# Optimization experiments

Measured on AMD Instinct MI355X. Metric: run time of the kernel, lower is better.

Reference implementation:

```python
import jax, jax.numpy as jnp
import numpy as np

HID = 128
CDIM = 128
NCH = 3
NDIM = 3


def _linear_params(key, fan_in, fan_out):
    kw, kb = jax.random.split(key)
    bound = 1.0 / np.sqrt(fan_in)
    W = jax.random.uniform(kw, (fan_in, fan_out), jnp.float32, -bound, bound)
    b = jax.random.uniform(kb, (fan_out,), jnp.float32, -bound, bound)
    return W, b


def setup_inputs() -> dict:
    key = jax.random.key(0)
    keys = jax.random.split(key, 12)
    p = jax.random.normal(keys[0], (32, 8192, NDIM), jnp.float32)
    W_pos, b_pos = _linear_params(keys[1], NDIM, 2 * HID)
    W0, b0 = _linear_params(keys[2], 2 * HID, HID)
    W1, b1 = _linear_params(keys[3], 2 * HID, HID)
    W2, b2 = _linear_params(keys[4], 2 * HID, HID)
    W3, b3 = _linear_params(keys[5], 2 * HID, HID)
    Wc, bc = _linear_params(keys[6], HID, CDIM)
    Wm0, bm0 = _linear_params(keys[7], CDIM, HID)
    Wm1, bm1 = _linear_params(keys[8], HID, HID)
    Wm2, bm2 = _linear_params(keys[9], HID, HID)
    Wp, bp = _linear_params(keys[10], HID, NCH * 3)
    return dict(p=p, W_pos=W_pos, b_pos=b_pos, W0=W0, b0=b0, W1=W1, b1=b1,
                W2=W2, b2=b2, W3=W3, b3=b3, Wc=Wc, bc=bc,
                Wm0=Wm0, bm0=bm0, Wm1=Wm1, bm1=bm1, Wm2=Wm2, bm2=bm2,
                Wp=Wp, bp=bp)


def _relu(x):
    return jnp.maximum(x, 0)


def _pool_cat(net):
    # max over points (dim=1), broadcast back and concat on features
    pooled = jnp.max(net, axis=1, keepdims=True)
    pooled = jnp.broadcast_to(pooled, net.shape)
    return jnp.concatenate([net, pooled], axis=2)  # [B, T, 2*hid]


def reference(p, W_pos, b_pos, W0, b0, W1, b1, W2, b2, W3, b3,
              Wc, bc, Wm0, bm0, Wm1, bm1, Wm2, bm2, Wp, bp):
    net = p @ W_pos + b_pos                      # [B, T, 2*hid]
    net = _relu(net) @ W0 + b0                   # [B, T, hid]
    net = _relu(_pool_cat(net)) @ W1 + b1        # [B, T, hid]
    net = _relu(_pool_cat(net)) @ W2 + b2        # [B, T, hid]
    net = _relu(_pool_cat(net)) @ W3 + b3        # [B, T, hid]
    net = jnp.max(net, axis=1)                   # [B, hid]
    net = _relu(net) @ Wc + bc                   # [B, c_dim]
    net = _relu(net) @ Wm0 + bm0
    net = _relu(net) @ Wm1 + bm1
    net = _relu(net) @ Wm2 + bm2
    net = _relu(net) @ Wp + bp                   # [B, n_channels*3]
    return net
```

## Files before the change

kernel.cpp:

```cpp
#include <hip/hip_runtime.h>


using bf16x8 = __attribute__((ext_vector_type(8))) __bf16;
using u16x8  = __attribute__((ext_vector_type(8))) unsigned short;
using f32x4  = __attribute__((ext_vector_type(4))) float;

__device__ __forceinline__ unsigned short f2bf(float x) {
  __bf16 b = (__bf16)x;
  return __builtin_bit_cast(unsigned short, b);
}

__device__ __forceinline__ f32x4 mfma16(bf16x8 a, bf16x8 b, f32x4 c) {
  return __builtin_amdgcn_mfma_f32_16x16x32_bf16(a, b, c, 0, 0, 0);
}

union FragU { unsigned short us[8]; u16x8 u; bf16x8 v; };

__global__ __launch_bounds__(256) void k_pack_all(
    const float* __restrict__ W0, const float* __restrict__ W1,
    const float* __restrict__ W2, const float* __restrict__ W3,
    unsigned short* __restrict__ Wt) {
  const int blk = blockIdx.x, t = threadIdx.x;
  const float* src; int slot; unsigned short* dst;
  if (blk < 16)      { src = W0; slot = blk * 256 + t;        dst = Wt; }
  else if (blk < 24) { src = W1; slot = (blk - 16) * 256 + t; dst = Wt + 32768; }
  else if (blk < 32) { src = W2; slot = (blk - 24) * 256 + t; dst = Wt + 49152; }
  else               { src = W3; slot = (blk - 32) * 256 + t; dst = Wt + 65536; }
  const int ks = slot >> 9, rem = slot & 511;
  const int nt = rem >> 6, lane = rem & 63;
  const int n = nt * 16 + (lane & 15);
  const int kb = ks * 32 + ((lane >> 4) << 3);
  FragU fr;
#pragma unroll
  for (int j = 0; j < 8; ++j) fr.us[j] = f2bf(src[(kb + j) * 128 + n]);
  reinterpret_cast<u16x8*>(dst)[slot] = fr.u;
}

__global__ __launch_bounds__(256) void k_layer0(
    const float* __restrict__ p, const float* __restrict__ Wpos,
    const float* __restrict__ bpos, const float* __restrict__ b0,
    const unsigned short* __restrict__ Wt0, unsigned short* __restrict__ h,
    float* __restrict__ pm) {
  __shared__ unsigned short wlsb[1024];
  __shared__ float pmaxs[2][128];
  const int t = threadIdx.x, blk = blockIdx.x;

  {
    const int m = t;
    const int phi = ((m >> 4) >> 1) * 32 + (((m & 15) >> 2) << 3) +
                    (((m >> 4) & 1) << 2) + (m & 3);
    ushort4 wv;
    wv.x = f2bf(Wpos[phi]);       wv.y = f2bf(Wpos[256 + phi]);
    wv.z = f2bf(Wpos[512 + phi]); wv.w = f2bf(bpos[phi]);
    *reinterpret_cast<ushort4*>(&wlsb[m * 4]) = wv;
  }
  __syncthreads();

  const int w = t >> 6, lane = t & 63, g = lane >> 4, c = lane & 15;
  const int rowg = w >> 1, colg = w & 1;

  FragU pf[2];
#pragma unroll
  for (int mi = 0; mi < 2; ++mi) {
#pragma unroll
    for (int j = 0; j < 8; ++j) pf[mi].us[j] = 0;
    if (g == 0) {
      const int row = blk * 64 + rowg * 32 + mi * 16 + c;
      pf[mi].us[0] = f2bf(p[row * 3 + 0]);
      pf[mi].us[1] = f2bf(p[row * 3 + 1]);
      pf[mi].us[2] = f2bf(p[row * 3 + 2]);
      pf[mi].us[3] = (unsigned short)0x3F80;
    }
  }

  f32x4 acc[2][4];
#pragma unroll
  for (int mi = 0; mi < 2; ++mi)
#pragma unroll
    for (int ntl = 0; ntl < 4; ++ntl) acc[mi][ntl] = f32x4{0.f, 0.f, 0.f, 0.f};

  const bf16x8* Bf = reinterpret_cast<const bf16x8*>(Wt0);
  const f32x4 zz = {0.f, 0.f, 0.f, 0.f};

#pragma unroll
  for (int ks = 0; ks < 8; ++ks) {
    bf16x8 B[4];
#pragma unroll
    for (int ntl = 0; ntl < 4; ++ntl)
      B[ntl] = Bf[(ks * 8 + colg * 4 + ntl) * 64 + lane];

    FragU a1_0, a1_1;
#pragma unroll
    for (int j = 0; j < 8; ++j) { a1_0.us[j] = 0; a1_1.us[j] = 0; }
    if (g == 0) {
      const ushort4 wv0 = *reinterpret_cast<const ushort4*>(&wlsb[((2 * ks) * 16 + c) * 4]);
      const ushort4 wv1 = *reinterpret_cast<const ushort4*>(&wlsb[((2 * ks + 1) * 16 + c) * 4]);
      a1_0.us[0] = wv0.x; a1_0.us[1] = wv0.y; a1_0.us[2] = wv0.z; a1_0.us[3] = wv0.w;
      a1_1.us[0] = wv1.x; a1_1.us[1] = wv1.y; a1_1.us[2] = wv1.z; a1_1.us[3] = wv1.w;
    }

#pragma unroll
    for (int mi = 0; mi < 2; ++mi) {
      const f32x4 qe0 = mfma16(a1_0.v, pf[mi].v, zz);
      const f32x4 qe1 = mfma16(a1_1.v, pf[mi].v, zz);
      FragU af;
#pragma unroll
      for (int j = 0; j < 4; ++j) af.us[j] = f2bf(fmaxf(qe0[j], 0.f));
#pragma unroll
      for (int j = 0; j < 4; ++j) af.us[4 + j] = f2bf(fmaxf(qe1[j], 0.f));
#pragma unroll
      for (int ntl = 0; ntl < 4; ++ntl)
        acc[mi][ntl] = mfma16(B[ntl], af.v, acc[mi][ntl]);
    }
  }

  unsigned short* hout = h + (size_t)blk * 8192;
#pragma unroll
  for (int ntl = 0; ntl < 4; ++ntl) {
    const int ntg = colg * 4 + ntl;
    const float4 bb = *reinterpret_cast<const float4*>(&b0[ntg * 16 + g * 4]);
    float vm[4] = {0.f, 0.f, 0.f, 0.f};
#pragma unroll
    for (int mi = 0; mi < 2; ++mi) {
      const float v0 = fmaxf(acc[mi][ntl][0] + bb.x, 0.f);
      const float v1 = fmaxf(acc[mi][ntl][1] + bb.y, 0.f);
      const float v2 = fmaxf(acc[mi][ntl][2] + bb.z, 0.f);
      const float v3 = fmaxf(acc[mi][ntl][3] + bb.w, 0.f);
      vm[0] = fmaxf(vm[0], v0); vm[1] = fmaxf(vm[1], v1);
      vm[2] = fmaxf(vm[2], v2); vm[3] = fmaxf(vm[3], v3);
      ushort4 s4;
      s4.x = f2bf(v0); s4.y = f2bf(v1); s4.z = f2bf(v2); s4.w = f2bf(v3);
      const int slot = (rowg * 2 + mi) * 256 + (ntg >> 1) * 64 +
                       ((ntg & 1) * 2 + (g >> 1)) * 16 + c;
      *reinterpret_cast<ushort4*>(&hout[slot * 8 + (g & 1) * 4]) = s4;
    }
#pragma unroll
    for (int r = 0; r < 4; ++r) {
      vm[r] = fmaxf(vm[r], __shfl_xor(vm[r], 1, 64));
      vm[r] = fmaxf(vm[r], __shfl_xor(vm[r], 2, 64));
      vm[r] = fmaxf(vm[r], __shfl_xor(vm[r], 4, 64));
      vm[r] = fmaxf(vm[r], __shfl_xor(vm[r], 8, 64));
    }
    if (c == 0) {
#pragma unroll
      for (int r = 0; r < 4; ++r) pmaxs[rowg][ntg * 16 + g * 4 + r] = vm[r];
    }
  }
  __syncthreads();
  if (t < 128) pm[(size_t)blk * 128 + t] = fmaxf(pmaxs[0][t], pmaxs[1][t]);
}

__global__ __launch_bounds__(256) void k_layer(
    const unsigned short* __restrict__ Wta, const float* __restrict__ cvec,
    unsigned short* __restrict__ h, float* __restrict__ pm, int write_h) {
  __shared__ float pmaxs[2][128];
  const int t = threadIdx.x, blk = blockIdx.x;
  const int w = t >> 6, lane = t & 63, g = lane >> 4, c = lane & 15;
  const int rowg = w >> 1, colg = w & 1;
  const int b = blk >> 6;

  f32x4 acc[4][4];
#pragma unroll
  for (int mi = 0; mi < 4; ++mi)
#pragma unroll
    for (int ntl = 0; ntl < 4; ++ntl) acc[mi][ntl] = f32x4{0.f, 0.f, 0.f, 0.f};

  const u16x8* hblk = reinterpret_cast<const u16x8*>(h) + (size_t)blk * 2048;
  const bf16x8* Bf = reinterpret_cast<const bf16x8*>(Wta);
#pragma unroll
  for (int ks = 0; ks < 4; ++ks) {
    bf16x8 B[4];
#pragma unroll
    for (int ntl = 0; ntl < 4; ++ntl)
      B[ntl] = Bf[(ks * 8 + colg * 4 + ntl) * 64 + lane];
    FragU a[4];
#pragma unroll
    for (int mi = 0; mi < 4; ++mi)
      a[mi].u = hblk[(rowg * 4 + mi) * 256 + ks * 64 + lane];
#pragma unroll
    for (int mi = 0; mi < 4; ++mi)
#pragma unroll
      for (int ntl = 0; ntl < 4; ++ntl)
        acc[mi][ntl] = mfma16(B[ntl], a[mi].v, acc[mi][ntl]);
  }

  unsigned short* hout = h + (size_t)blk * 16384;
#pragma unroll
  for (int ntl = 0; ntl < 4; ++ntl) {
    const int ntg = colg * 4 + ntl;
    const float4 bb = *reinterpret_cast<const float4*>(&cvec[b * 128 + ntg * 16 + g * 4]);
    float vm[4] = {0.f, 0.f, 0.f, 0.f};
#pragma unroll
    for (int mi = 0; mi < 4; ++mi) {
      const float v0 = fmaxf(acc[mi][ntl][0] + bb.x, 0.f);
      const float v1 = fmaxf(acc[mi][ntl][1] + bb.y, 0.f);
      const float v2 = fmaxf(acc[mi][ntl][2] + bb.z, 0.f);
      const float v3 = fmaxf(acc[mi][ntl][3] + bb.w, 0.f);
      vm[0] = fmaxf(vm[0], v0); vm[1] = fmaxf(vm[1], v1);
      vm[2] = fmaxf(vm[2], v2); vm[3] = fmaxf(vm[3], v3);
      if (write_h) {
        ushort4 s4;
        s4.x = f2bf(v0); s4.y = f2bf(v1); s4.z = f2bf(v2); s4.w = f2bf(v3);
        const int slot = (rowg * 4 + mi) * 256 + (ntg >> 1) * 64 +
                         ((ntg & 1) * 2 + (g >> 1)) * 16 + c;
        *reinterpret_cast<ushort4*>(&hout[slot * 8 + (g & 1) * 4]) = s4;
      }
    }
#pragma unroll
    for (int r = 0; r < 4; ++r) {
      vm[r] = fmaxf(vm[r], __shfl_xor(vm[r], 1, 64));
      vm[r] = fmaxf(vm[r], __shfl_xor(vm[r], 2, 64));
      vm[r] = fmaxf(vm[r], __shfl_xor(vm[r], 4, 64));
      vm[r] = fmaxf(vm[r], __shfl_xor(vm[r], 8, 64));
    }
    if (c == 0) {
#pragma unroll
      for (int r = 0; r < 4; ++r) pmaxs[rowg][ntg * 16 + g * 4 + r] = vm[r];
    }
  }
  __syncthreads();
  if (t < 128) pm[(size_t)blk * 128 + t] = fmaxf(pmaxs[0][t], pmaxs[1][t]);
}

__global__ __launch_bounds__(256) void k_combine(
    const float* __restrict__ pm, const float* __restrict__ Wn,
    const float* __restrict__ bn, float* __restrict__ cout, int nper) {
  const int b = blockIdx.x, t = threadIdx.x;
  const int f = t & 127, half = t >> 7;
  __shared__ float part[2][128];
  __shared__ float rm[128];
  const int hn = nper >> 1;
  float m = 0.f;
  for (int i = half * hn; i < half * hn + hn; ++i)
    m = fmaxf(m, pm[(size_t)(b * nper + i) * 128 + f]);
  part[half][f] = m;
  __syncthreads();
  if (t < 128) rm[f] = fmaxf(part[0][f], part[1][f]);
  __syncthreads();
  float s = 0.f;
  for (int q = half * 64; q < half * 64 + 64; ++q)
    s += rm[q] * Wn[(128 + q) * 128 + f];
  part[half][f] = s;
  __syncthreads();
  if (t < 128) cout[b * 128 + f] = part[0][f] + part[1][f] + bn[f];
}

__global__ __launch_bounds__(256) void k_final(
    const float* __restrict__ pm3, int nper,
    const float* __restrict__ Wc,  const float* __restrict__ bc,
    const float* __restrict__ Wm0, const float* __restrict__ bm0,
    const float* __restrict__ Wm1, const float* __restrict__ bm1,
    const float* __restrict__ Wm2, const float* __restrict__ bm2,
    const float* __restrict__ Wp,  const float* __restrict__ bp,
    float* __restrict__ out) {
  const int b = blockIdx.x, t = threadIdx.x;
  const int f = t & 127, half = t >> 7;
  __shared__ float part[2][128];
  __shared__ float x[128];
  const int hn = nper >> 1;
  float m = 0.f;
  for (int i = half * hn; i < half * hn + hn; ++i)
    m = fmaxf(m, pm3[(size_t)(b * nper + i) * 128 + f]);
  part[half][f] = m;
  __syncthreads();
  if (t < 128) x[f] = fmaxf(part[0][f], part[1][f]);
  __syncthreads();

  const float* Ws[4] = {Wc, Wm0, Wm1, Wm2};
  const float* bs[4] = {bc, bm0, bm1, bm2};
#pragma unroll
  for (int L = 0; L < 4; ++L) {
    float s = 0.f;
    for (int q = half * 64; q < half * 64 + 64; ++q)
      s += x[q] * Ws[L][q * 128 + f];
    part[half][f] = s;
    __syncthreads();
    if (t < 128) x[f] = fmaxf(part[0][f] + part[1][f] + bs[L][f], 0.f);
    __syncthreads();
  }
  if (t < 9) {
    float s = bp[t];
    for (int q = 0; q < 128; ++q) s += x[q] * Wp[q * 9 + t];
    out[b * 9 + t] = s;
  }
}

extern "C" void kernel_launch(void* const* d_in, const int* in_sizes, int n_in,
                              void* d_out, int out_size, void* d_ws, size_t ws_size,
                              hipStream_t stream) {
  const float *p = nullptr, *Wpos = nullptr, *bpos = nullptr;
  const float *Wp = nullptr, *bp = nullptr;
  const float *W256[4] = {}; int nW256 = 0;
  const float *W128[4] = {}; int nW128 = 0;
  const float *B128[8] = {}; int nB128 = 0;
  for (int i = 0; i < n_in; ++i) {
    const float* q = (const float*)d_in[i];
    switch (in_sizes[i]) {
      case 786432: p = q; break;
      case 768:    Wpos = q; break;
      case 256:    bpos = q; break;
      case 1152:   Wp = q; break;
      case 9:      bp = q; break;
      case 32768:  if (nW256 < 4) W256[nW256++] = q; break;
      case 16384:  if (nW128 < 4) W128[nW128++] = q; break;
      case 128:    if (nB128 < 8) B128[nB128++] = q; break;
      default: break;
    }
  }
  const float *W0 = W256[0], *W1 = W256[1], *W2 = W256[2], *W3 = W256[3];
  const float *Wc = W128[0], *Wm0 = W128[1], *Wm1 = W128[2], *Wm2 = W128[3];
  const float *b0 = B128[0], *b1 = B128[1], *b2 = B128[2], *b3 = B128[3];
  const float *bc = B128[4], *bm0 = B128[5], *bm1 = B128[6], *bm2 = B128[7];
  float* out = (float*)d_out;

  char* ws = (char*)d_ws;
  float* pm = (float*)ws;
  float* cv = (float*)(ws + 2097152);
  unsigned short* Wt = (unsigned short*)(ws + 2097152 + 16384);
  unsigned short* Wt0 = Wt;
  unsigned short* Wt1 = Wt + 32768;
  unsigned short* Wt2 = Wt + 49152;
  unsigned short* Wt3 = Wt + 65536;
  unsigned short* h = Wt + 81920;

  k_pack_all<<<40, 256, 0, stream>>>(W0, W1, W2, W3, Wt);
  k_layer0<<<4096, 256, 0, stream>>>(p, Wpos, bpos, b0, Wt0, h, pm);
  k_combine<<<32, 256, 0, stream>>>(pm, W1, b1, cv, 128);
  k_layer<<<2048, 256, 0, stream>>>(Wt1, cv, h, pm, 1);
  k_combine<<<32, 256, 0, stream>>>(pm, W2, b2, cv, 64);
  k_layer<<<2048, 256, 0, stream>>>(Wt2, cv, h, pm, 1);
  k_combine<<<32, 256, 0, stream>>>(pm, W3, b3, cv, 64);
  k_layer<<<2048, 256, 0, stream>>>(Wt3, cv, h, pm, 0);
  k_final<<<32, 256, 0, stream>>>(pm, 64, Wc, bc, Wm0, bm0, Wm1, bm1, Wm2, bm2, Wp, bp, out);
}
```

Baseline: 179.9 us.

## Restructure hidden-layer kernel to 512-thread tiles with LDS-staged coalesced output

The k_layer kernel now uses 512-thread blocks covering 256 points each, with every wave computing all 128 output columns for 32 rows, so the B fragments are shared across two row tiles. The epilogue stages the bf16 results through a padded LDS buffer so each lane writes full 16-byte vectors in the fragment layout the next layer reads, instead of scattered 8-byte stores. The per-block column max is reduced across 8 waves, and the combine and final kernels are passed half as many partial maxima per batch. This should cut redundant weight loads and improve store coalescing, at the cost of more LDS traffic, higher register pressure, and an extra LDS round trip per tile.

```diff
diff --git a/kernel.cpp b/kernel.cpp
--- a/kernel.cpp
+++ b/kernel.cpp
@@ -150,76 +150,97 @@
   if (t < 128) pm[(size_t)blk * 128 + t] = fmaxf(pmaxs[0][t], pmaxs[1][t]);
 }
 
-__global__ __launch_bounds__(256) void k_layer(
+__device__ __forceinline__ void epilogue512(
+    unsigned short* hsw, float (*pmaxs)[128], const f32x4 (&acc)[2][8],
+    const float (&bias)[8], int t, int blk, unsigned short* __restrict__ h,
+    float* __restrict__ pm, bool write_h) {
+  const int w = t >> 6, lane = t & 63, g = lane >> 4, c = lane & 15;
+  float colmax[8];
+#pragma unroll
+  for (int nt = 0; nt < 8; ++nt) colmax[nt] = 0.f;
+
+  if (write_h) {
+    u16x8* hout = reinterpret_cast<u16x8*>(h) + (size_t)blk * 4096;
+#pragma unroll
+    for (int mi = 0; mi < 2; ++mi) {
+#pragma unroll
+      for (int nt = 0; nt < 8; ++nt) {
+#pragma unroll
+        for (int r = 0; r < 4; ++r) {
+          const float v = fmaxf(acc[mi][nt][r] + bias[nt], 0.f);
+          colmax[nt] = fmaxf(colmax[nt], v);
+          hsw[(g * 4 + r) * 136 + nt * 16 + c] = f2bf(v);
+        }
+      }
+#pragma unroll
+      for (int s = 0; s < 4; ++s) {
+        const u16x8 val =
+            *reinterpret_cast<const u16x8*>(&hsw[(lane & 15) * 136 + s * 32 + 8 * g]);
+        hout[(w * 2 + mi) * 256 + s * 64 + lane] = val;
+      }
+    }
+  } else {
+#pragma unroll
+    for (int mi = 0; mi < 2; ++mi)
+#pragma unroll
+      for (int nt = 0; nt < 8; ++nt)
+#pragma unroll
+        for (int r = 0; r < 4; ++r)
+          colmax[nt] = fmaxf(colmax[nt], acc[mi][nt][r] + bias[nt]);
+  }
+
+#pragma unroll
+  for (int nt = 0; nt < 8; ++nt) {
+    colmax[nt] = fmaxf(colmax[nt], __shfl_xor(colmax[nt], 16, 64));
+    colmax[nt] = fmaxf(colmax[nt], __shfl_xor(colmax[nt], 32, 64));
+  }
+  if (lane < 16) {
+#pragma unroll
+    for (int nt = 0; nt < 8; ++nt) pmaxs[w][nt * 16 + c] = colmax[nt];
+  }
+  __syncthreads();
+  if (t < 128) {
+    float m = pmaxs[0][t];
+#pragma unroll
+    for (int i = 1; i < 8; ++i) m = fmaxf(m, pmaxs[i][t]);
+    pm[(size_t)blk * 128 + t] = m;
+  }
+}
+
+__global__ __launch_bounds__(512, 4) void k_layer(
     const unsigned short* __restrict__ Wta, const float* __restrict__ cvec,
     unsigned short* __restrict__ h, float* __restrict__ pm, int write_h) {
-  __shared__ float pmaxs[2][128];
+  __shared__ unsigned short HS[8 * 2176];
+  __shared__ float pmaxs[8][128];
   const int t = threadIdx.x, blk = blockIdx.x;
-  const int w = t >> 6, lane = t & 63, g = lane >> 4, c = lane & 15;
-  const int rowg = w >> 1, colg = w & 1;
-  const int b = blk >> 6;
-
-  f32x4 acc[4][4];
-#pragma unroll
-  for (int mi = 0; mi < 4; ++mi)
-#pragma unroll
-    for (int ntl = 0; ntl < 4; ++ntl) acc[mi][ntl] = f32x4{0.f, 0.f, 0.f, 0.f};
-
-  const u16x8* hblk = reinterpret_cast<const u16x8*>(h) + (size_t)blk * 2048;
+  const int w = t >> 6, lane = t & 63, c = lane & 15;
+  const int b = blk >> 5;
+
+  float bias[8];
+#pragma unroll
+  for (int nt = 0; nt < 8; ++nt) bias[nt] = cvec[b * 128 + nt * 16 + c];
+
+  f32x4 acc[2][8];
+#pragma unroll
+  for (int mi = 0; mi < 2; ++mi)
+#pragma unroll
+    for (int nt = 0; nt < 8; ++nt) acc[mi][nt] = f32x4{0.f, 0.f, 0.f, 0.f};
+
+  const u16x8* hbase = reinterpret_cast<const u16x8*>(h) + (size_t)blk * 4096;
   const bf16x8* Bf = reinterpret_cast<const bf16x8*>(Wta);
 #pragma unroll
   for (int ks = 0; ks < 4; ++ks) {
-    bf16x8 B[4];
-#pragma unroll
-    for (int ntl = 0; ntl < 4; ++ntl)
-      B[ntl] = Bf[(ks * 8 + colg * 4 + ntl) * 64 + lane];
-    FragU a[4];
-#pragma unroll
-    for (int mi = 0; mi < 4; ++mi)
-      a[mi].u = hblk[(rowg * 4 + mi) * 256 + ks * 64 + lane];
-#pragma unroll
-    for (int mi = 0; mi < 4; ++mi)
-#pragma unroll
-      for (int ntl = 0; ntl < 4; ++ntl)
-        acc[mi][ntl] = mfma16(B[ntl], a[mi].v, acc[mi][ntl]);
-  }
-
-  unsigned short* hout = h + (size_t)blk * 16384;
-#pragma unroll
-  for (int ntl = 0; ntl < 4; ++ntl) {
-    const int ntg = colg * 4 + ntl;
-    const float4 bb = *reinterpret_cast<const float4*>(&cvec[b * 128 + ntg * 16 + g * 4]);
-    float vm[4] = {0.f, 0.f, 0.f, 0.f};
-#pragma unroll
-    for (int mi = 0; mi < 4; ++mi) {
-      const float v0 = fmaxf(acc[mi][ntl][0] + bb.x, 0.f);
-      const float v1 = fmaxf(acc[mi][ntl][1] + bb.y, 0.f);
-      const float v2 = fmaxf(acc[mi][ntl][2] + bb.z, 0.f);
-      const float v3 = fmaxf(acc[mi][ntl][3] + bb.w, 0.f);
-      vm[0] = fmaxf(vm[0], v0); vm[1] = fmaxf(vm[1], v1);
-      vm[2] = fmaxf(vm[2], v2); vm[3] = fmaxf(vm[3], v3);
-      if (write_h) {
-        ushort4 s4;
-        s4.x = f2bf(v0); s4.y = f2bf(v1); s4.z = f2bf(v2); s4.w = f2bf(v3);
-        const int slot = (rowg * 4 + mi) * 256 + (ntg >> 1) * 64 +
-                         ((ntg & 1) * 2 + (g >> 1)) * 16 + c;
-        *reinterpret_cast<ushort4*>(&hout[slot * 8 + (g & 1) * 4]) = s4;
-      }
-    }
-#pragma unroll
-    for (int r = 0; r < 4; ++r) {
-      vm[r] = fmaxf(vm[r], __shfl_xor(vm[r], 1, 64));
-      vm[r] = fmaxf(vm[r], __shfl_xor(vm[r], 2, 64));
-      vm[r] = fmaxf(vm[r], __shfl_xor(vm[r], 4, 64));
-      vm[r] = fmaxf(vm[r], __shfl_xor(vm[r], 8, 64));
-    }
-    if (c == 0) {
-#pragma unroll
-      for (int r = 0; r < 4; ++r) pmaxs[rowg][ntg * 16 + g * 4 + r] = vm[r];
-    }
-  }
-  __syncthreads();
-  if (t < 128) pm[(size_t)blk * 128 + t] = fmaxf(pmaxs[0][t], pmaxs[1][t]);
+    FragU a0, a1;
+    a0.u = hbase[(w * 2 + 0) * 256 + ks * 64 + lane];
+    a1.u = hbase[(w * 2 + 1) * 256 + ks * 64 + lane];
+#pragma unroll
+    for (int nt = 0; nt < 8; ++nt) {
+      const bf16x8 B = Bf[(ks * 8 + nt) * 64 + lane];
+      acc[0][nt] = mfma16(a0.v, B, acc[0][nt]);
+      acc[1][nt] = mfma16(a1.v, B, acc[1][nt]);
+    }
+  }
+  epilogue512(&HS[w * 2176], pmaxs, acc, bias, t, blk, h, pm, write_h != 0);
 }
 
 __global__ __launch_bounds__(256) void k_combine(
@@ -326,10 +347,10 @@
   k_pack_all<<<40, 256, 0, stream>>>(W0, W1, W2, W3, Wt);
   k_layer0<<<4096, 256, 0, stream>>>(p, Wpos, bpos, b0, Wt0, h, pm);
   k_combine<<<32, 256, 0, stream>>>(pm, W1, b1, cv, 128);
-  k_layer<<<2048, 256, 0, stream>>>(Wt1, cv, h, pm, 1);
-  k_combine<<<32, 256, 0, stream>>>(pm, W2, b2, cv, 64);
-  k_layer<<<2048, 256, 0, stream>>>(Wt2, cv, h, pm, 1);
-  k_combine<<<32, 256, 0, stream>>>(pm, W3, b3, cv, 64);
-  k_layer<<<2048, 256, 0, stream>>>(Wt3, cv, h, pm, 0);
-  k_final<<<32, 256, 0, stream>>>(pm, 64, Wc, bc, Wm0, bm0, Wm1, bm1, Wm2, bm2, Wp, bp, out);
-}
+  k_layer<<<1024, 512, 0, stream>>>(Wt1, cv, h, pm, 1);
+  k_combine<<<32, 256, 0, stream>>>(pm, W2, b2, cv, 32);
+  k_layer<<<1024, 512, 0, stream>>>(Wt2, cv, h, pm, 1);
+  k_combine<<<32, 256, 0, stream>>>(pm, W3, b3, cv, 32);
+  k_layer<<<1024, 512, 0, stream>>>(Wt3, cv, h, pm, 0);
+  k_final<<<32, 256, 0, stream>>>(pm, 32, Wc, bc, Wm0, bm0, Wm1, bm1, Wm2, bm2, Wp, bp, out);
+}
```

New measurement: 173.1 us. 3.8% less time.
